# Kernel tuning notes

Hardware: AMD Instinct MI355X
Metric: run time of the kernel (lower is better)

## Reference

```python
import jax, jax.numpy as jnp
import numpy as np

IN_F, T_IN, T_OUT = 8, 96, 32
B = 4096


def _lstm(x, Wih, Whh, b):
    """Standard LSTM (torch gate order i,f,g,o), batch_first. x: [B,T,I] -> [B,T,H].
    Variational dropout with p=0 (eval mode) is identity, so omitted."""
    Bsz = x.shape[0]
    H = Whh.shape[1]
    # precompute input contribution for all timesteps: [B,T,4H]
    xg = jnp.einsum('bti,gi->btg', x, Wih) + b

    def step(carry, xt):
        h, c = carry
        g = xt + h @ Whh.T  # [B,4H]
        i, f, gg, o = jnp.split(g, 4, axis=-1)
        c = jax.nn.sigmoid(f) * c + jax.nn.sigmoid(i) * jnp.tanh(gg)
        h = jax.nn.sigmoid(o) * jnp.tanh(c)
        return (h, c), h

    h0 = jnp.zeros((Bsz, H), x.dtype)
    _, ys = jax.lax.scan(step, (h0, h0), jnp.swapaxes(xg, 0, 1))
    return jnp.swapaxes(ys, 0, 1)


def setup_inputs() -> dict:
    key = jax.random.key(0)
    ks = jax.random.split(key, 16)
    s = 0.1  # init scale
    return {
        'x': jax.random.normal(ks[0], (B, T_IN, IN_F), jnp.float32),
        'e1_Wih': s * jax.random.normal(ks[1], (256, IN_F), jnp.float32),
        'e1_Whh': s * jax.random.normal(ks[2], (256, 64), jnp.float32),
        'e1_b': s * jax.random.normal(ks[3], (256,), jnp.float32),
        'e2_Wih': s * jax.random.normal(ks[4], (4, 64), jnp.float32),
        'e2_Whh': s * jax.random.normal(ks[5], (4, 1), jnp.float32),
        'e2_b': s * jax.random.normal(ks[6], (4,), jnp.float32),
        'd1_Wih': s * jax.random.normal(ks[7], (64, 1), jnp.float32),
        'd1_Whh': s * jax.random.normal(ks[8], (64, 16), jnp.float32),
        'd1_b': s * jax.random.normal(ks[9], (64,), jnp.float32),
        'd2_Wih': s * jax.random.normal(ks[10], (4, 16), jnp.float32),
        'd2_Whh': s * jax.random.normal(ks[11], (4, 1), jnp.float32),
        'd2_b': s * jax.random.normal(ks[12], (4,), jnp.float32),
        'fc1_W': s * jax.random.normal(ks[13], (32, T_IN + T_OUT), jnp.float32),
        'fc1_b': s * jax.random.normal(ks[13], (32,), jnp.float32),
        'fc2_W': s * jax.random.normal(ks[14], (T_OUT, 32), jnp.float32),
        'fc2_b': s * jax.random.normal(ks[15], (T_OUT,), jnp.float32),
    }


def reference(x, e1_Wih, e1_Whh, e1_b, e2_Wih, e2_Whh, e2_b,
              d1_Wih, d1_Whh, d1_b, d2_Wih, d2_Whh, d2_b,
              fc1_W, fc1_b, fc2_W, fc2_b):
    # Encoder: LSTM(in->64) -> LSTM(64->1) -> ReLU
    h = _lstm(x, e1_Wih, e1_Whh, e1_b)
    h = _lstm(h, e2_Wih, e2_Whh, e2_b)
    enc_out = jax.nn.relu(h)  # [B, T_IN, 1]
    # Auxiliary: last T_OUT steps of invocation column (col 0)
    x_aux = x[:, -T_OUT:, 0:1]  # [B, T_OUT, 1]
    dec_in = jnp.concatenate([enc_out, x_aux], axis=1)  # [B, T_IN+T_OUT, 1]
    # Decoder: LSTM(1->16) -> LSTM(16->1)
    d = _lstm(dec_in, d1_Wih, d1_Whh, d1_b)
    d = _lstm(d, d2_Wih, d2_Whh, d2_b)  # [B, T_IN+T_OUT, 1]
    # FC head over the flattened time dim
    flat = d.reshape(-1, T_IN + T_OUT)
    out = flat @ fc1_W.T + fc1_b
    out = out @ fc2_W.T + fc2_b
    return out  # [B, T_OUT]
```

## Files before the change

### kernel.cpp

```cpp
#include <hip/hip_runtime.h>
#include <hip/hip_bf16.h>

typedef __attribute__((ext_vector_type(8))) short bf16x8;
typedef __attribute__((ext_vector_type(4))) float f32x4;

__device__ __forceinline__ float sigm(float x) {
    return __builtin_amdgcn_rcpf(1.0f + __expf(-x));
}
__device__ __forceinline__ float tanh_(float x) {
    float e = __expf(2.0f * x);
    return 1.0f - 2.0f * __builtin_amdgcn_rcpf(e + 1.0f);
}
__device__ __forceinline__ ushort f2bf(float f) {
    uint u = __float_as_uint(f);
    u = u + 0x7FFFu + ((u >> 16) & 1u);
    return (ushort)(u >> 16);
}
__device__ __forceinline__ float bf2f(ushort s) { return __uint_as_float(((uint)s) << 16); }
__device__ __forceinline__ float sel4(f32x4 a, int k) {
    float lo = (k & 1) ? a[1] : a[0];
    float hi = (k & 1) ? a[3] : a[2];
    return (k & 2) ? hi : lo;
}
__device__ __forceinline__ float sel4v(float a0, float a1, float a2, float a3, int s) {
    float lo = (s & 1) ? a1 : a0;
    float hi = (s & 1) ? a3 : a2;
    return (s & 2) ? hi : lo;
}

__global__ __launch_bounds__(512) __attribute__((amdgpu_waves_per_eu(2, 2)))
void k1_e1(
    const float* __restrict__ x,
    const float* __restrict__ e1_Wih, const float* __restrict__ e1_Whh, const float* __restrict__ e1_b,
    const float* __restrict__ e2_Wih, const float* __restrict__ e2_b,
    float* __restrict__ pe2)
{
    __shared__ float x_s[16 * 768];
    __shared__ __align__(16) ushort h_hi[2][16 * 72];
    __shared__ __align__(16) ushort h_lo[2][16 * 72];
    __shared__ __align__(16) ushort x2_s[2][16 * 40];

    const int t = threadIdx.x;
    const int bBase = blockIdx.x * 16;
    const int l = t & 63, wv = t >> 6;
    const int q = l & 15, sub = l >> 4;
    const int u_loc = q >> 2, g = q & 3;

    for (int i = t; i < 16 * 768; i += 512) x_s[i] = x[(size_t)bBase * 768 + i];

    auto loadW = [&](const float* rowbase, int k0, bool valid, bf16x8& hi8, bf16x8& lo8) {
        float f[8];
        if (valid) {
            float4 v0 = ((const float4*)(rowbase + k0))[0];
            float4 v1 = ((const float4*)(rowbase + k0))[1];
            f[0]=v0.x; f[1]=v0.y; f[2]=v0.z; f[3]=v0.w;
            f[4]=v1.x; f[5]=v1.y; f[6]=v1.z; f[7]=v1.w;
        } else {
            #pragma unroll
            for (int j = 0; j < 8; ++j) f[j] = 0.f;
        }
        #pragma unroll
        for (int j = 0; j < 8; ++j) {
            ushort h = f2bf(f[j]);
            hi8[j] = (short)h;
            lo8[j] = (short)f2bf(f[j] - bf2f(h));
        }
    };
    auto loadTileB = [&](int T, bf16x8& Bh0, bf16x8& Bh1, bf16x8& Bl0, bf16x8& Bl1, bf16x8& B2) {
        const bool isE2 = (T == 16);
        const bool valid = !isE2 || (u_loc == 0);
        const int wrow = isE2 ? g : (g * 64 + T * 4 + u_loc);
        const float* rowp = isE2 ? (e2_Wih + (size_t)wrow * 64) : (e1_Whh + (size_t)wrow * 64);
        loadW(rowp, sub * 8,      valid, Bh0, Bl0);
        loadW(rowp, 32 + sub * 8, valid, Bh1, Bl1);
        #pragma unroll
        for (int j = 0; j < 8; ++j) B2[j] = 0;
        if (!isE2) {
            if (sub < 3) {
                const float* wr = e1_Wih + (size_t)wrow * 8;
                #pragma unroll
                for (int j = 0; j < 8; ++j) {
                    float f = wr[j];
                    ushort h = f2bf(f);
                    B2[j] = (sub < 2) ? (short)h : (short)f2bf(f - bf2f(h));
                }
            } else {
                float bb = e1_b[wrow];
                ushort h = f2bf(bb);
                B2[0] = (short)h; B2[1] = (short)f2bf(bb - bf2f(h));
            }
        } else if (valid && sub == 3) {
            float bb = e2_b[g];
            ushort h = f2bf(bb);
            B2[0] = (short)h; B2[1] = (short)f2bf(bb - bf2f(h));
        }
    };

    const int T0 = 2 * wv, T1 = 2 * wv + 1;
    bf16x8 B0h0, B0h1, B0l0, B0l1, B0x;
    bf16x8 B1h0, B1h1, B1l0, B1l1, B1x;
    bf16x8 B2h0, B2h1, B2l0, B2l1, B2x;
    loadTileB(T0, B0h0, B0h1, B0l0, B0l1, B0x);
    loadTileB(T1, B1h0, B1h1, B1l0, B1l1, B1x);
    if (wv == 7) loadTileB(16, B2h0, B2h1, B2l0, B2l1, B2x);

    __syncthreads();

    for (int i = t; i < 16 * 72; i += 512) { h_hi[0][i] = 0; h_lo[0][i] = 0; }
    {
        int bb = t >> 5, pos = t & 31;
        ushort v0 = 0;
        if (pos < 24) {
            float xv = x_s[bb * 768 + (pos & 7)];
            ushort hi = f2bf(xv);
            v0 = (pos < 8) ? hi : (pos < 16) ? f2bf(xv - bf2f(hi)) : hi;
        } else if (pos == 24 || pos == 25) v0 = 0x3F80;
        x2_s[0][bb * 40 + pos] = v0;
        x2_s[1][bb * 40 + pos] = (pos == 24 || pos == 25) ? (ushort)0x3F80 : (ushort)0;
    }

    float c0r = 0.f, c1r = 0.f;
    __syncthreads();

    #pragma unroll 1
    for (int ts = 0; ts < 96; ++ts) {
        const int p = ts & 1, pn = p ^ 1;

        bf16x8 Ah0 = *(const bf16x8*)&h_hi[p][q * 72 + sub * 8];
        bf16x8 Ah1 = *(const bf16x8*)&h_hi[p][q * 72 + 32 + sub * 8];
        bf16x8 Al0 = *(const bf16x8*)&h_lo[p][q * 72 + sub * 8];
        bf16x8 Al1 = *(const bf16x8*)&h_lo[p][q * 72 + 32 + sub * 8];
        bf16x8 A2v = *(const bf16x8*)&x2_s[p][q * 40 + sub * 8];

        f32x4 a0 = {0.f,0.f,0.f,0.f}, e0 = {0.f,0.f,0.f,0.f};
        a0 = __builtin_amdgcn_mfma_f32_16x16x32_bf16(Ah0, B0h0, a0, 0, 0, 0);
        a0 = __builtin_amdgcn_mfma_f32_16x16x32_bf16(Al0, B0h0, a0, 0, 0, 0);
        a0 = __builtin_amdgcn_mfma_f32_16x16x32_bf16(Ah0, B0l0, a0, 0, 0, 0);
        e0 = __builtin_amdgcn_mfma_f32_16x16x32_bf16(Ah1, B0h1, e0, 0, 0, 0);
        e0 = __builtin_amdgcn_mfma_f32_16x16x32_bf16(Al1, B0h1, e0, 0, 0, 0);
        e0 = __builtin_amdgcn_mfma_f32_16x16x32_bf16(Ah1, B0l1, e0, 0, 0, 0);
        e0 = __builtin_amdgcn_mfma_f32_16x16x32_bf16(A2v, B0x,  e0, 0, 0, 0);

        f32x4 a1 = {0.f,0.f,0.f,0.f}, e1 = {0.f,0.f,0.f,0.f};
        a1 = __builtin_amdgcn_mfma_f32_16x16x32_bf16(Ah0, B1h0, a1, 0, 0, 0);
        a1 = __builtin_amdgcn_mfma_f32_16x16x32_bf16(Al0, B1h0, a1, 0, 0, 0);
        a1 = __builtin_amdgcn_mfma_f32_16x16x32_bf16(Ah0, B1l0, a1, 0, 0, 0);
        e1 = __builtin_amdgcn_mfma_f32_16x16x32_bf16(Ah1, B1h1, e1, 0, 0, 0);
        e1 = __builtin_amdgcn_mfma_f32_16x16x32_bf16(Al1, B1h1, e1, 0, 0, 0);
        e1 = __builtin_amdgcn_mfma_f32_16x16x32_bf16(Ah1, B1l1, e1, 0, 0, 0);
        e1 = __builtin_amdgcn_mfma_f32_16x16x32_bf16(A2v, B1x,  e1, 0, 0, 0);

        if (wv == 7) {
            f32x4 a2 = {0.f,0.f,0.f,0.f}, e2 = {0.f,0.f,0.f,0.f};
            a2 = __builtin_amdgcn_mfma_f32_16x16x32_bf16(Ah0, B2h0, a2, 0, 0, 0);
            a2 = __builtin_amdgcn_mfma_f32_16x16x32_bf16(Al0, B2h0, a2, 0, 0, 0);
            a2 = __builtin_amdgcn_mfma_f32_16x16x32_bf16(Ah0, B2l0, a2, 0, 0, 0);
            e2 = __builtin_amdgcn_mfma_f32_16x16x32_bf16(Ah1, B2h1, e2, 0, 0, 0);
            e2 = __builtin_amdgcn_mfma_f32_16x16x32_bf16(Al1, B2h1, e2, 0, 0, 0);
            e2 = __builtin_amdgcn_mfma_f32_16x16x32_bf16(Ah1, B2l1, e2, 0, 0, 0);
            e2 = __builtin_amdgcn_mfma_f32_16x16x32_bf16(A2v, B2x,  e2, 0, 0, 0);
            if (ts > 0 && u_loc == 0) {
                f32x4 acc2 = a2 + e2;
                #pragma unroll
                for (int i = 0; i < 4; ++i)
                    pe2[((size_t)(ts - 1) * 4096 + bBase + 4 * sub + i) * 4 + g] = acc2[i];
            }
        }

        {
            f32x4 acc = a0 + e0;
            float own = sel4(acc, g);
            float r1 = __shfl_xor(sel4(acc, g ^ 1), 1);
            float r2 = __shfl_xor(sel4(acc, g ^ 2), 2);
            float r3 = __shfl_xor(sel4(acc, g ^ 3), 3);
            float pi = sel4v(own, r1, r2, r3, g);
            float pf = sel4v(own, r1, r2, r3, g ^ 1);
            float pg = sel4v(own, r1, r2, r3, g ^ 2);
            float po = sel4v(own, r1, r2, r3, g ^ 3);
            c0r = fmaf(sigm(pf), c0r, sigm(pi) * tanh_(pg));
            float hv = sigm(po) * tanh_(c0r);
            int idx = (4 * sub + g) * 72 + T0 * 4 + u_loc;
            ushort hh = f2bf(hv);
            h_hi[pn][idx] = hh;
            h_lo[pn][idx] = f2bf(hv - bf2f(hh));
        }
        {
            f32x4 acc = a1 + e1;
            float own = sel4(acc, g);
            float r1 = __shfl_xor(sel4(acc, g ^ 1), 1);
            float r2 = __shfl_xor(sel4(acc, g ^ 2), 2);
            float r3 = __shfl_xor(sel4(acc, g ^ 3), 3);
            float pi = sel4v(own, r1, r2, r3, g);
            float pf = sel4v(own, r1, r2, r3, g ^ 1);
            float pg = sel4v(own, r1, r2, r3, g ^ 2);
            float po = sel4v(own, r1, r2, r3, g ^ 3);
            c1r = fmaf(sigm(pf), c1r, sigm(pi) * tanh_(pg));
            float hv = sigm(po) * tanh_(c1r);
            int idx = (4 * sub + g) * 72 + T1 * 4 + u_loc;
            ushort hh = f2bf(hv);
            h_hi[pn][idx] = hh;
            h_lo[pn][idx] = f2bf(hv - bf2f(hh));
        }

        if (ts < 95) {
            int bb = t >> 5, pos = t & 31;
            if (pos < 24) {
                float xv = x_s[bb * 768 + (ts + 1) * 8 + (pos & 7)];
                ushort hi = f2bf(xv);
                x2_s[pn][bb * 40 + pos] = (pos < 8) ? hi : (pos < 16) ? f2bf(xv - bf2f(hi)) : hi;
            }
        }
        __syncthreads();
    }

    if (wv == 7) {
        bf16x8 Ah0 = *(const bf16x8*)&h_hi[0][q * 72 + sub * 8];
        bf16x8 Ah1 = *(const bf16x8*)&h_hi[0][q * 72 + 32 + sub * 8];
        bf16x8 Al0 = *(const bf16x8*)&h_lo[0][q * 72 + sub * 8];
        bf16x8 Al1 = *(const bf16x8*)&h_lo[0][q * 72 + 32 + sub * 8];
        bf16x8 A2v = *(const bf16x8*)&x2_s[0][q * 40 + sub * 8];
        f32x4 a2 = {0.f,0.f,0.f,0.f}, e2 = {0.f,0.f,0.f,0.f};
        a2 = __builtin_amdgcn_mfma_f32_16x16x32_bf16(Ah0, B2h0, a2, 0, 0, 0);
        a2 = __builtin_amdgcn_mfma_f32_16x16x32_bf16(Al0, B2h0, a2, 0, 0, 0);
        a2 = __builtin_amdgcn_mfma_f32_16x16x32_bf16(Ah0, B2l0, a2, 0, 0, 0);
        e2 = __builtin_amdgcn_mfma_f32_16x16x32_bf16(Ah1, B2h1, e2, 0, 0, 0);
        e2 = __builtin_amdgcn_mfma_f32_16x16x32_bf16(Al1, B2h1, e2, 0, 0, 0);
        e2 = __builtin_amdgcn_mfma_f32_16x16x32_bf16(Ah1, B2l1, e2, 0, 0, 0);
        e2 = __builtin_amdgcn_mfma_f32_16x16x32_bf16(A2v, B2x,  e2, 0, 0, 0);
        if (u_loc == 0) {
            f32x4 acc2 = a2 + e2;
            #pragma unroll
            for (int i = 0; i < 4; ++i)
                pe2[((size_t)95 * 4096 + bBase + 4 * sub + i) * 4 + g] = acc2[i];
        }
    }
}

__global__ __launch_bounds__(64) __attribute__((amdgpu_waves_per_eu(2, 2)))
void k2_e2(const float* __restrict__ pe2, const float* __restrict__ e2_Whh,
           const float* __restrict__ x, float* __restrict__ dec_in)
{
    const int b = blockIdx.x * 64 + threadIdx.x;
    const float w0 = e2_Whh[0], w1 = e2_Whh[1], w2 = e2_Whh[2], w3 = e2_Whh[3];
    const float4* pp = (const float4*)pe2;
    float4 buf[16];
    #pragma unroll
    for (int j = 0; j < 16; ++j) buf[j] = pp[(size_t)j * 4096 + b];
    float h = 0.f, c = 0.f;
    #pragma unroll
    for (int ts = 0; ts < 96; ++ts) {
        float4 g4 = buf[ts & 15];
        if (ts + 16 < 96) buf[ts & 15] = pp[(size_t)(ts + 16) * 4096 + b];
        float gi = fmaf(h, w0, g4.x);
        float gf = fmaf(h, w1, g4.y);
        float gg = fmaf(h, w2, g4.z);
        float go = fmaf(h, w3, g4.w);
        c = fmaf(sigm(gf), c, sigm(gi) * tanh_(gg));
        h = sigm(go) * tanh_(c);
        dec_in[(size_t)ts * 4096 + b] = fmaxf(h, 0.f);
    }
    #pragma unroll 8
    for (int j = 0; j < 32; ++j)
        dec_in[(size_t)(96 + j) * 4096 + b] = x[(size_t)b * 768 + (64 + j) * 8];
}

__global__ __launch_bounds__(256, 2) void k3_dec(
    const float* __restrict__ dec_in,
    const float* __restrict__ d1_Wih, const float* __restrict__ d1_Whh, const float* __restrict__ d1_b,
    const float* __restrict__ d2_Wih, const float* __restrict__ d2_b,
    const float* __restrict__ d2_Whh,
    const float* __restrict__ fc1_W, const float* __restrict__ fc1_b,
    const float* __restrict__ fc2_W, const float* __restrict__ fc2_b,
    float* __restrict__ out)
{
    __shared__ float din_s[16 * 129];
    __shared__ float h_lds[16][16];
    __shared__ float pd2_s[16 * 516];
    __shared__ float d2h_s[16 * 132];
    __shared__ float mid_s[16 * 36];

    const int t = threadIdx.x;
    const int w = t >> 6, lane = t & 63;
    const int qq4 = lane >> 4, u = lane & 15;
    const int row = w * 4 + qq4;
    const size_t bBase = (size_t)blockIdx.x * 16;

    for (int i = t; i < 2048; i += 256) {
        int ts = i >> 4, rr = i & 15;
        din_s[rr * 129 + ts] = dec_in[(size_t)ts * 4096 + bBase + rr];
    }

    float wih_g[4], bg[4], whh_g[4][16], d2w[16];
    #pragma unroll
    for (int g = 0; g < 4; ++g) {
        wih_g[g] = d1_Wih[g * 16 + u];
        bg[g]    = d1_b[g * 16 + u];
        const float4* wp = (const float4*)(d1_Whh + (size_t)(g * 16 + u) * 16);
        #pragma unroll
        for (int k4 = 0; k4 < 4; ++k4) {
            float4 v = wp[k4];
            whh_g[g][4*k4+0] = v.x; whh_g[g][4*k4+1] = v.y;
            whh_g[g][4*k4+2] = v.z; whh_g[g][4*k4+3] = v.w;
        }
    }
    {
        const float4* wp = (const float4*)(d2_Wih + (size_t)(u & 3) * 16);
        #pragma unroll
        for (int k4 = 0; k4 < 4; ++k4) {
            float4 v = wp[k4];
            d2w[4*k4+0] = v.x; d2w[4*k4+1] = v.y; d2w[4*k4+2] = v.z; d2w[4*k4+3] = v.w;
        }
    }
    const float d2bias = d2_b[u & 3];

    float h = 0.f, c = 0.f;
    __syncthreads();

    float hv[16];
    for (int ts = 0; ts < 128; ++ts) {
        float xv = din_s[row * 129 + ts];
        float p0 = fmaf(xv, wih_g[0], bg[0]);
        float p1 = fmaf(xv, wih_g[1], bg[1]);
        float p2 = fmaf(xv, wih_g[2], bg[2]);
        float p3 = fmaf(xv, wih_g[3], bg[3]);
        if (ts > 0) {
            const float4* hp = (const float4*)&h_lds[row][0];
            #pragma unroll
            for (int k4 = 0; k4 < 4; ++k4) {
                float4 v = hp[k4];
                hv[4*k4+0] = v.x; hv[4*k4+1] = v.y; hv[4*k4+2] = v.z; hv[4*k4+3] = v.w;
            }
            #pragma unroll
            for (int k = 0; k < 16; ++k) {
                p0 = fmaf(hv[k], whh_g[0][k], p0);
                p1 = fmaf(hv[k], whh_g[1][k], p1);
                p2 = fmaf(hv[k], whh_g[2][k], p2);
                p3 = fmaf(hv[k], whh_g[3][k], p3);
            }
            if (u < 4) {
                float a = d2bias;
                #pragma unroll
                for (int k = 0; k < 16; ++k) a = fmaf(hv[k], d2w[k], a);
                pd2_s[row * 516 + (ts - 1) * 4 + u] = a;
            }
        }
        c = fmaf(sigm(p1), c, sigm(p0) * tanh_(p2));
        h = sigm(p3) * tanh_(c);
        h_lds[row][u] = h;
    }
    {
        const float4* hp = (const float4*)&h_lds[row][0];
        #pragma unroll
        for (int k4 = 0; k4 < 4; ++k4) {
            float4 v = hp[k4];
            hv[4*k4+0] = v.x; hv[4*k4+1] = v.y; hv[4*k4+2] = v.z; hv[4*k4+3] = v.w;
        }
        if (u < 4) {
            float a = d2bias;
            #pragma unroll
            for (int k = 0; k < 16; ++k) a = fmaf(hv[k], d2w[k], a);
            pd2_s[row * 516 + 127 * 4 + u] = a;
        }
    }
    __syncthreads();

    {
        const float w0 = d2_Whh[0], w1 = d2_Whh[1], w2 = d2_Whh[2], w3 = d2_Whh[3];
        if (t < 16) {
            float h2 = 0.f, c2 = 0.f;
            #pragma unroll 8
            for (int ts = 0; ts < 128; ++ts) {
                float4 g4 = *(const float4*)&pd2_s[t * 516 + ts * 4];
                float gi = fmaf(h2, w0, g4.x);
                float gf = fmaf(h2, w1, g4.y);
                float gg = fmaf(h2, w2, g4.z);
                float go = fmaf(h2, w3, g4.w);
                c2 = fmaf(sigm(gf), c2, sigm(gi) * tanh_(gg));
                h2 = sigm(go) * tanh_(c2);
                d2h_s[t * 132 + ts] = h2;
            }
        }
    }
    __syncthreads();

    {
        const int bb = t >> 4, o = t & 15;
        float acc0 = fc1_b[o], acc1 = fc1_b[o + 16];
        const float4* wa = (const float4*)(fc1_W + (size_t)o * 128);
        const float4* wb = (const float4*)(fc1_W + (size_t)(o + 16) * 128);
        const float4* fp = (const float4*)&d2h_s[bb * 132];
        #pragma unroll
        for (int k4 = 0; k4 < 32; ++k4) {
            float4 f = fp[k4], va = wa[k4], vb = wb[k4];
            acc0 = fmaf(f.x, va.x, acc0); acc0 = fmaf(f.y, va.y, acc0);
            acc0 = fmaf(f.z, va.z, acc0); acc0 = fmaf(f.w, va.w, acc0);
            acc1 = fmaf(f.x, vb.x, acc1); acc1 = fmaf(f.y, vb.y, acc1);
            acc1 = fmaf(f.z, vb.z, acc1); acc1 = fmaf(f.w, vb.w, acc1);
        }
        mid_s[bb * 36 + o] = acc0;
        mid_s[bb * 36 + o + 16] = acc1;
        __syncthreads();
        float o0 = fc2_b[o], o1 = fc2_b[o + 16];
        const float4* va2 = (const float4*)(fc2_W + (size_t)o * 32);
        const float4* vb2 = (const float4*)(fc2_W + (size_t)(o + 16) * 32);
        const float4* mp = (const float4*)&mid_s[bb * 36];
        #pragma unroll
        for (int k4 = 0; k4 < 8; ++k4) {
            float4 m = mp[k4], va = va2[k4], vb = vb2[k4];
            o0 = fmaf(m.x, va.x, o0); o0 = fmaf(m.y, va.y, o0);
            o0 = fmaf(m.z, va.z, o0); o0 = fmaf(m.w, va.w, o0);
            o1 = fmaf(m.x, vb.x, o1); o1 = fmaf(m.y, vb.y, o1);
            o1 = fmaf(m.z, vb.z, o1); o1 = fmaf(m.w, vb.w, o1);
        }
        out[(bBase + bb) * 32 + o] = o0;
        out[(bBase + bb) * 32 + o + 16] = o1;
    }
}

extern "C" void kernel_launch(void* const* d_in, const int* in_sizes, int n_in,
                              void* d_out, int out_size, void* d_ws, size_t ws_size,
                              hipStream_t stream) {
    const float* x      = (const float*)d_in[0];
    const float* e1_Wih = (const float*)d_in[1];
    const float* e1_Whh = (const float*)d_in[2];
    const float* e1_b   = (const float*)d_in[3];
    const float* e2_Wih = (const float*)d_in[4];
    const float* e2_Whh = (const float*)d_in[5];
    const float* e2_b   = (const float*)d_in[6];
    const float* d1_Wih = (const float*)d_in[7];
    const float* d1_Whh = (const float*)d_in[8];
    const float* d1_b   = (const float*)d_in[9];
    const float* d2_Wih = (const float*)d_in[10];
    const float* d2_Whh = (const float*)d_in[11];
    const float* d2_b   = (const float*)d_in[12];
    const float* fc1_W  = (const float*)d_in[13];
    const float* fc1_b  = (const float*)d_in[14];
    const float* fc2_W  = (const float*)d_in[15];
    const float* fc2_b  = (const float*)d_in[16];
    float* out = (float*)d_out;

    float* ws     = (float*)d_ws;
    float* pe2    = ws;
    float* dec_in = ws + 1572864;

    hipLaunchKernelGGL(k1_e1, dim3(256), dim3(512), 0, stream,
                       x, e1_Wih, e1_Whh, e1_b, e2_Wih, e2_b, pe2);
    hipLaunchKernelGGL(k2_e2, dim3(64), dim3(64), 0, stream, pe2, e2_Whh, x, dec_in);
    hipLaunchKernelGGL(k3_dec, dim3(256), dim3(256), 0, stream,
                       dec_in, d1_Wih, d1_Whh, d1_b, d2_Wih, d2_b, d2_Whh,
                       fc1_W, fc1_b, fc2_W, fc2_b, out);
}
```

Measured before the change: 175.9 us.

## Fuse e2 recurrence into encoder kernel with 8-row blocks and LDS gate staging

Folds the second encoder LSTM (previously a separate kernel reading gate pre-activations from global memory) into the first encoder kernel. Gate pre-activations now go to shared memory, and one wave runs the scalar recurrence at the end. Each block now handles 8 batch rows instead of 16, doubling the grid to 512 blocks and raising waves_per_eu to 4, so the MFMA tiles are half empty. The decoder's d2 recurrence also gains a small register prefetch buffer for its shared-memory gate loads.

```diff
diff --git a/kernel.cpp b/kernel.cpp
--- a/kernel.cpp
+++ b/kernel.cpp
@@ -28,25 +28,27 @@
     return (s & 2) ? hi : lo;
 }
 
-__global__ __launch_bounds__(512) __attribute__((amdgpu_waves_per_eu(2, 2)))
-void k1_e1(
+__global__ __launch_bounds__(512) __attribute__((amdgpu_waves_per_eu(4, 4)))
+void k1_enc(
     const float* __restrict__ x,
     const float* __restrict__ e1_Wih, const float* __restrict__ e1_Whh, const float* __restrict__ e1_b,
     const float* __restrict__ e2_Wih, const float* __restrict__ e2_b,
-    float* __restrict__ pe2)
+    const float* __restrict__ e2_Whh,
+    float* __restrict__ dec_in)
 {
-    __shared__ float x_s[16 * 768];
+    __shared__ float x_s[8 * 768];
     __shared__ __align__(16) ushort h_hi[2][16 * 72];
     __shared__ __align__(16) ushort h_lo[2][16 * 72];
     __shared__ __align__(16) ushort x2_s[2][16 * 40];
+    __shared__ __align__(16) float pe2_s[96 * 8 * 4];
 
     const int t = threadIdx.x;
-    const int bBase = blockIdx.x * 16;
+    const int bBase = blockIdx.x * 8;
     const int l = t & 63, wv = t >> 6;
     const int q = l & 15, sub = l >> 4;
     const int u_loc = q >> 2, g = q & 3;
 
-    for (int i = t; i < 16 * 768; i += 512) x_s[i] = x[(size_t)bBase * 768 + i];
+    for (int i = t; i < 8 * 768; i += 512) x_s[i] = x[(size_t)bBase * 768 + i];
 
     auto loadW = [&](const float* rowbase, int k0, bool valid, bf16x8& hi8, bf16x8& lo8) {
         float f[8];
@@ -109,14 +111,16 @@
     for (int i = t; i < 16 * 72; i += 512) { h_hi[0][i] = 0; h_lo[0][i] = 0; }
     {
         int bb = t >> 5, pos = t & 31;
-        ushort v0 = 0;
-        if (pos < 24) {
-            float xv = x_s[bb * 768 + (pos & 7)];
-            ushort hi = f2bf(xv);
-            v0 = (pos < 8) ? hi : (pos < 16) ? f2bf(xv - bf2f(hi)) : hi;
-        } else if (pos == 24 || pos == 25) v0 = 0x3F80;
+        ushort v0 = 0, v1 = 0;
+        if (bb < 8) {
+            if (pos < 24) {
+                float xv = x_s[bb * 768 + (pos & 7)];
+                ushort hi = f2bf(xv);
+                v0 = (pos < 8) ? hi : (pos < 16) ? f2bf(xv - bf2f(hi)) : hi;
+            } else if (pos == 24 || pos == 25) { v0 = 0x3F80; v1 = 0x3F80; }
+        }
         x2_s[0][bb * 40 + pos] = v0;
-        x2_s[1][bb * 40 + pos] = (pos == 24 || pos == 25) ? (ushort)0x3F80 : (ushort)0;
+        x2_s[1][bb * 40 + pos] = v1;
     }
 
     float c0r = 0.f, c1r = 0.f;
@@ -159,11 +163,11 @@
             e2 = __builtin_amdgcn_mfma_f32_16x16x32_bf16(Al1, B2h1, e2, 0, 0, 0);
             e2 = __builtin_amdgcn_mfma_f32_16x16x32_bf16(Ah1, B2l1, e2, 0, 0, 0);
             e2 = __builtin_amdgcn_mfma_f32_16x16x32_bf16(A2v, B2x,  e2, 0, 0, 0);
-            if (ts > 0 && u_loc == 0) {
+            if (ts > 0 && u_loc == 0 && sub < 2) {
                 f32x4 acc2 = a2 + e2;
                 #pragma unroll
                 for (int i = 0; i < 4; ++i)
-                    pe2[((size_t)(ts - 1) * 4096 + bBase + 4 * sub + i) * 4 + g] = acc2[i];
+                    pe2_s[((size_t)(ts - 1) * 8 + 4 * sub + i) * 4 + g] = acc2[i];
             }
         }
 
@@ -204,7 +208,7 @@
 
         if (ts < 95) {
             int bb = t >> 5, pos = t & 31;
-            if (pos < 24) {
+            if (bb < 8 && pos < 24) {
                 float xv = x_s[bb * 768 + (ts + 1) * 8 + (pos & 7)];
                 ushort hi = f2bf(xv);
                 x2_s[pn][bb * 40 + pos] = (pos < 8) ? hi : (pos < 16) ? f2bf(xv - bf2f(hi)) : hi;
@@ -227,41 +231,38 @@
         e2 = __builtin_amdgcn_mfma_f32_16x16x32_bf16(Al1, B2h1, e2, 0, 0, 0);
         e2 = __builtin_amdgcn_mfma_f32_16x16x32_bf16(Ah1, B2l1, e2, 0, 0, 0);
         e2 = __builtin_amdgcn_mfma_f32_16x16x32_bf16(A2v, B2x,  e2, 0, 0, 0);
-        if (u_loc == 0) {
+        if (u_loc == 0 && sub < 2) {
             f32x4 acc2 = a2 + e2;
             #pragma unroll
             for (int i = 0; i < 4; ++i)
-                pe2[((size_t)95 * 4096 + bBase + 4 * sub + i) * 4 + g] = acc2[i];
-        }
-    }
-}
-
-__global__ __launch_bounds__(64) __attribute__((amdgpu_waves_per_eu(2, 2)))
-void k2_e2(const float* __restrict__ pe2, const float* __restrict__ e2_Whh,
-           const float* __restrict__ x, float* __restrict__ dec_in)
-{
-    const int b = blockIdx.x * 64 + threadIdx.x;
-    const float w0 = e2_Whh[0], w1 = e2_Whh[1], w2 = e2_Whh[2], w3 = e2_Whh[3];
-    const float4* pp = (const float4*)pe2;
-    float4 buf[16];
-    #pragma unroll
-    for (int j = 0; j < 16; ++j) buf[j] = pp[(size_t)j * 4096 + b];
-    float h = 0.f, c = 0.f;
-    #pragma unroll
-    for (int ts = 0; ts < 96; ++ts) {
-        float4 g4 = buf[ts & 15];
-        if (ts + 16 < 96) buf[ts & 15] = pp[(size_t)(ts + 16) * 4096 + b];
-        float gi = fmaf(h, w0, g4.x);
-        float gf = fmaf(h, w1, g4.y);
-        float gg = fmaf(h, w2, g4.z);
-        float go = fmaf(h, w3, g4.w);
-        c = fmaf(sigm(gf), c, sigm(gi) * tanh_(gg));
-        h = sigm(go) * tanh_(c);
-        dec_in[(size_t)ts * 4096 + b] = fmaxf(h, 0.f);
-    }
-    #pragma unroll 8
-    for (int j = 0; j < 32; ++j)
-        dec_in[(size_t)(96 + j) * 4096 + b] = x[(size_t)b * 768 + (64 + j) * 8];
+                pe2_s[((size_t)95 * 8 + 4 * sub + i) * 4 + g] = acc2[i];
+        }
+    }
+    __syncthreads();
+
+    if (wv == 0 && l < 8) {
+        const float w0 = e2_Whh[0], w1 = e2_Whh[1], w2 = e2_Whh[2], w3 = e2_Whh[3];
+        const float4* pp4 = (const float4*)pe2_s;
+        float4 buf[4];
+        #pragma unroll
+        for (int j = 0; j < 4; ++j) buf[j] = pp4[j * 8 + l];
+        float h = 0.f, c = 0.f;
+        #pragma unroll
+        for (int ts = 0; ts < 96; ++ts) {
+            float4 g4 = buf[ts & 3];
+            if (ts + 4 < 96) buf[ts & 3] = pp4[(ts + 4) * 8 + l];
+            float gi = fmaf(h, w0, g4.x);
+            float gf = fmaf(h, w1, g4.y);
+            float gg = fmaf(h, w2, g4.z);
+            float go = fmaf(h, w3, g4.w);
+            c = fmaf(sigm(gf), c, sigm(gi) * tanh_(gg));
+            h = sigm(go) * tanh_(c);
+            dec_in[(size_t)ts * 4096 + bBase + l] = fmaxf(h, 0.f);
+        }
+        #pragma unroll 8
+        for (int j = 0; j < 32; ++j)
+            dec_in[(size_t)(96 + j) * 4096 + bBase + l] = x_s[l * 768 + (64 + j) * 8];
+    }
 }
 
 __global__ __launch_bounds__(256, 2) void k3_dec(
@@ -367,10 +368,14 @@
     {
         const float w0 = d2_Whh[0], w1 = d2_Whh[1], w2 = d2_Whh[2], w3 = d2_Whh[3];
         if (t < 16) {
+            float4 dbuf[4];
+            #pragma unroll
+            for (int j = 0; j < 4; ++j) dbuf[j] = *(const float4*)&pd2_s[t * 516 + j * 4];
             float h2 = 0.f, c2 = 0.f;
-            #pragma unroll 8
+            #pragma unroll
             for (int ts = 0; ts < 128; ++ts) {
-                float4 g4 = *(const float4*)&pd2_s[t * 516 + ts * 4];
+                float4 g4 = dbuf[ts & 3];
+                if (ts + 4 < 128) dbuf[ts & 3] = *(const float4*)&pd2_s[t * 516 + (ts + 4) * 4];
                 float gi = fmaf(h2, w0, g4.x);
                 float gf = fmaf(h2, w1, g4.y);
                 float gg = fmaf(h2, w2, g4.z);
@@ -439,13 +444,10 @@
     const float* fc2_b  = (const float*)d_in[16];
     float* out = (float*)d_out;
 
-    float* ws     = (float*)d_ws;
-    float* pe2    = ws;
-    float* dec_in = ws + 1572864;
-
-    hipLaunchKernelGGL(k1_e1, dim3(256), dim3(512), 0, stream,
-                       x, e1_Wih, e1_Whh, e1_b, e2_Wih, e2_b, pe2);
-    hipLaunchKernelGGL(k2_e2, dim3(64), dim3(64), 0, stream, pe2, e2_Whh, x, dec_in);
+    float* dec_in = (float*)d_ws;
+
+    hipLaunchKernelGGL(k1_enc, dim3(512), dim3(512), 0, stream,
+                       x, e1_Wih, e1_Whh, e1_b, e2_Wih, e2_b, e2_Whh, dec_in);
     hipLaunchKernelGGL(k3_dec, dim3(256), dim3(256), 0, stream,
                        dec_in, d1_Wih, d1_Whh, d1_b, d2_Wih, d2_b, d2_Whh,
                        fc1_W, fc1_b, fc2_W, fc2_b, out);
```

After: 230.2 us. +30.9%, slower.
